# Optimization experiments

Hardware: AMD Instinct MI355X
Metric: run time of the kernel (lower is better)

## Reference

```python
import jax, jax.numpy as jnp
import numpy as np

B, T, D, KDIM = 256, 512, 256, 256

def setup_inputs() -> dict:
    key = jax.random.key(0)
    k1, k2, k3 = jax.random.split(key, 3)
    inputs = jax.random.normal(k1, (B, T, D), dtype=jnp.float32)
    # glorot-style scaling for stability of the recurrence
    U = jax.random.normal(k2, (D, KDIM), dtype=jnp.float32) * (1.0 / np.sqrt(D))
    W = jax.random.normal(k3, (KDIM, KDIM), dtype=jnp.float32) * (1.0 / np.sqrt(KDIM))
    b = jnp.zeros((KDIM,), dtype=jnp.float32)
    return {"inputs": inputs, "U": U, "W": W, "b": b}

def reference(inputs, U, W, b):
    # vanilla RNN: h_t = tanh(x_t U + h_{t-1} W + b); returns final hidden state
    xU = jnp.einsum('btd,dk->btk', inputs, U) + b  # precompute input projection [B,T,K]

    def step(h, xu_t):
        h = jnp.tanh(xu_t + h @ W)
        return h, None

    h0 = jnp.zeros((inputs.shape[0], W.shape[0]), dtype=inputs.dtype)
    h_final, _ = jax.lax.scan(step, h0, jnp.swapaxes(xU, 0, 1))  # scan over time
    # original keras code keeps a singleton time axis on the state: [B,1,K]
    return h_final[:, None, :]
```

## Files before the change

### kernel.cpp

```cpp
#include <hip/hip_runtime.h>
#include <hip/hip_bf16.h>


typedef _Float16 half8_t __attribute__((ext_vector_type(8)));
typedef _Float16 half2_t __attribute__((ext_vector_type(2)));
typedef float    float4_t __attribute__((ext_vector_type(4)));

#define MFMA16(a, b, c) __builtin_amdgcn_mfma_f32_16x16x32_f16((a), (b), (c), 0, 0, 0)

__device__ __forceinline__ half2_t pk_h2(float a, float b) {
    auto r = __builtin_amdgcn_cvt_pkrtz(a, b);
    return __builtin_bit_cast(half2_t, r);
}

__device__ __forceinline__ float fast_tanh(float x) {
    float e = __builtin_amdgcn_exp2f(2.8853900817779268f * x);
    return 1.0f - 2.0f * __builtin_amdgcn_rcpf(e + 1.0f);
}

__device__ __forceinline__ void lds_barrier() {
    __builtin_amdgcn_sched_barrier(0);
    asm volatile("s_waitcnt lgkmcnt(0)" ::: "memory");
    __builtin_amdgcn_s_barrier();
    __builtin_amdgcn_sched_barrier(0);
}

__global__ void transpose_u(const float* __restrict__ U, _Float16* __restrict__ Ut) {
    int id = blockIdx.x * 256 + threadIdx.x;
    int d = id >> 8, n = id & 255;
    Ut[n * 264 + d] = (_Float16)U[id];
}

__global__ __launch_bounds__(256, 2) void xu_gemm(
    const float* __restrict__ x,
    const _Float16* __restrict__ Ut,
    const float* __restrict__ bias,
    half2_t* __restrict__ xu)
{
    __shared__ char lds[61440];
    const int tid = threadIdx.x;
    const int lane = tid & 63, w = tid >> 6, l15 = lane & 15, q = lane >> 4;
    const int bx = blockIdx.x;
    const size_t m0 = (size_t)bx * 128;

    float4 ar[4];
    uint4  br[4];

    auto loadA = [&](int it) {
#pragma unroll
        for (int i = 0; i < 4; ++i) {
            int u = tid + 256 * i, row = u >> 3, seg = u & 7;
            ar[i] = *(const float4*)(x + (m0 + row) * 256 + it * 32 + seg * 4);
        }
    };
    auto loadB = [&](int it) {
#pragma unroll
        for (int i = 0; i < 4; ++i) {
            int u = tid + 256 * i, p = u >> 2, seg = u & 3;
            int c = 32 * (p >> 5) + 2 * (p & 15) + ((p >> 4) & 1);
            br[i] = *(const uint4*)((const char*)Ut + c * 528 + it * 64 + seg * 16);
        }
    };
    auto writeAB = [&](int s) {
        char* As = lds + s * 10240;
        char* Bs = lds + 20480 + s * 20480;
#pragma unroll
        for (int i = 0; i < 4; ++i) {
            int u = tid + 256 * i, row = u >> 3, seg = u & 7;
            half2_t p0 = pk_h2(ar[i].x, ar[i].y);
            half2_t p1 = pk_h2(ar[i].z, ar[i].w);
            uint2 v;
            v.x = __builtin_bit_cast(unsigned, p0);
            v.y = __builtin_bit_cast(unsigned, p1);
            *(uint2*)(As + row * 80 + seg * 8) = v;
        }
#pragma unroll
        for (int i = 0; i < 4; ++i) {
            int u = tid + 256 * i, p = u >> 2, seg = u & 3;
            *(uint4*)(Bs + p * 80 + seg * 16) = br[i];
        }
    };

    float4_t acc[32];
#pragma unroll
    for (int i = 0; i < 32; ++i) { acc[i][0] = 0.f; acc[i][1] = 0.f; acc[i][2] = 0.f; acc[i][3] = 0.f; }

    loadA(0); loadB(0); writeAB(0);
    __syncthreads();

    for (int it = 0; it < 8; ++it) {
        if (it < 7) { loadA(it + 1); loadB(it + 1); }
        const char* As = lds + (it & 1) * 10240;
        const char* Bs = lds + 20480 + (it & 1) * 20480;
        half8_t af[2];
#pragma unroll
        for (int ms = 0; ms < 2; ++ms)
            af[ms] = *(const half8_t*)(As + (32 * w + 16 * ms + l15) * 80 + q * 16);
#pragma unroll
        for (int ns = 0; ns < 16; ++ns) {
            half8_t bf = *(const half8_t*)(Bs + (16 * ns + l15) * 80 + q * 16);
            acc[ns * 2 + 0] = MFMA16(af[0], bf, acc[ns * 2 + 0]);
            acc[ns * 2 + 1] = MFMA16(af[1], bf, acc[ns * 2 + 1]);
        }
        if (it < 7) writeAB((it + 1) & 1);
        __syncthreads();
    }

#pragma unroll
    for (int ms = 0; ms < 2; ++ms)
#pragma unroll
        for (int j = 0; j < 8; ++j) {
            const int c = 32 * j + 2 * l15;
            const float2 bb = *(const float2*)(bias + c);
#pragma unroll
            for (int i = 0; i < 4; ++i) {
                float v0 = acc[(2 * j) * 2 + ms][i] + bb.x;
                float v1 = acc[(2 * j + 1) * 2 + ms][i] + bb.y;
                half2_t p = pk_h2(v0, v1);
                int m_g = bx * 128 + 32 * w + 16 * ms + q * 4 + i;
                xu[(size_t)m_g * 128 + (c >> 1)] = p;
            }
        }
}

__global__ __launch_bounds__(512, 2) void rnn_scan(
    const half2_t* __restrict__ xu,
    const float* __restrict__ W,
    float* __restrict__ out)
{
    __shared__ char lds[16896];
    const int tid = threadIdx.x;
    const int lane = tid & 63, w = tid >> 6, l15 = lane & 15, q = lane >> 4;
    const int blk = blockIdx.x;
    const int c0 = 32 * w + 2 * l15;

    half8_t wf[2][8];
#pragma unroll
    for (int tt = 0; tt < 2; ++tt)
#pragma unroll
        for (int c = 0; c < 8; ++c) {
            half8_t f;
#pragma unroll
            for (int j = 0; j < 8; ++j) {
                int k = 32 * c + q * 8 + j;
                f[j] = (_Float16)W[k * 256 + c0 + tt];
            }
            wf[tt][c] = f;
        }

    for (int i = tid; i < 16896 / 4; i += 512) ((int*)lds)[i] = 0;

    const int rowg0 = 16 * blk + q * 4;
    const int colh = c0 >> 1;

    half2_t xr[4][4];
#pragma unroll
    for (int p = 0; p < 4; ++p)
#pragma unroll
        for (int i = 0; i < 4; ++i)
            xr[p][i] = xu[((size_t)(rowg0 + i) * 512 + p) * 128 + colh];

    __syncthreads();

    char* const hbuf0 = (char*)lds;
    char* const hbuf1 = (char*)lds + 8448;

    for (int t4 = 0; t4 < 512; t4 += 4) {
#pragma unroll
        for (int p = 0; p < 4; ++p) {
            const int t = t4 + p;

            const char* hcur = (t & 1) ? hbuf1 : hbuf0;
            half8_t af[8];
#pragma unroll
            for (int c = 0; c < 8; ++c)
                af[c] = *(const half8_t*)(hcur + l15 * 528 + c * 64 + q * 16);

            float4_t a0a, a1a, a0b, a1b;
#pragma unroll
            for (int i = 0; i < 4; ++i) {
                a0a[i] = (float)xr[p][i][0];
                a1a[i] = (float)xr[p][i][1];
                a0b[i] = 0.f; a1b[i] = 0.f;
            }

            const int tn = (t + 4 <= 511) ? (t + 4) : 511;
#pragma unroll
            for (int i = 0; i < 4; ++i)
                xr[p][i] = xu[((size_t)(rowg0 + i) * 512 + tn) * 128 + colh];

#pragma unroll
            for (int c = 0; c < 4; ++c) {
                a0a = MFMA16(af[2 * c],     wf[0][2 * c],     a0a);
                a1a = MFMA16(af[2 * c],     wf[1][2 * c],     a1a);
                a0b = MFMA16(af[2 * c + 1], wf[0][2 * c + 1], a0b);
                a1b = MFMA16(af[2 * c + 1], wf[1][2 * c + 1], a1b);
            }

            if (t == 511) {
#pragma unroll
                for (int i = 0; i < 4; ++i) {
                    float v0 = fast_tanh(a0a[i] + a0b[i]);
                    float v1 = fast_tanh(a1a[i] + a1b[i]);
                    float2 st; st.x = v0; st.y = v1;
                    *(float2*)(&out[(rowg0 + i) * 256 + c0]) = st;
                }
            } else {
                char* hnext = ((t + 1) & 1) ? hbuf1 : hbuf0;
#pragma unroll
                for (int i = 0; i < 4; ++i) {
                    float v0 = fast_tanh(a0a[i] + a0b[i]);
                    float v1 = fast_tanh(a1a[i] + a1b[i]);
                    *(half2_t*)(hnext + (q * 4 + i) * 528 + c0 * 2) = pk_h2(v0, v1);
                }
            }
            lds_barrier();
        }
    }
}

extern "C" void kernel_launch(void* const* d_in, const int* in_sizes, int n_in,
                              void* d_out, int out_size, void* d_ws, size_t ws_size,
                              hipStream_t stream) {
    const float* x = (const float*)d_in[0];
    const float* U = (const float*)d_in[1];
    const float* W = (const float*)d_in[2];
    const float* b = (const float*)d_in[3];
    float* out = (float*)d_out;

    char* ws = (char*)d_ws;
    _Float16* Ut = (_Float16*)ws;
    half2_t*  xu = (half2_t*)(ws + 262144);

    transpose_u<<<256, 256, 0, stream>>>(U, Ut);
    xu_gemm<<<1024, 256, 0, stream>>>(x, Ut, b, xu);
    rnn_scan<<<16, 512, 0, stream>>>(xu, W, out);
}
```

Measured before the change: 521.1 us.

## Split RNN scan across 16 waves with one output column per lane

Doubles the scan block from 512 to 1024 threads, so each wave owns 16 output columns instead of 32. Each lane now computes a single column, which halves the MFMA chain per wave per timestep (4+4 instead of 8+8) and halves the W fragments held in registers. The aim is to shorten the serial per-step critical path of the recurrence. The cost is a barrier across twice as many waves each step, and narrower 16-bit LDS stores and xu loads.

After: 581.4 us. 1.12x slower.

```diff
diff --git a/kernel.cpp b/kernel.cpp
--- a/kernel.cpp
+++ b/kernel.cpp
@@ -123,8 +123,8 @@
         }
 }
 
-__global__ __launch_bounds__(512, 2) void rnn_scan(
-    const half2_t* __restrict__ xu,
+__global__ __launch_bounds__(1024, 4) void rnn_scan(
+    const _Float16* __restrict__ xu,
     const float* __restrict__ W,
     float* __restrict__ out)
 {
@@ -132,33 +132,30 @@
     const int tid = threadIdx.x;
     const int lane = tid & 63, w = tid >> 6, l15 = lane & 15, q = lane >> 4;
     const int blk = blockIdx.x;
-    const int c0 = 32 * w + 2 * l15;
-
-    half8_t wf[2][8];
-#pragma unroll
-    for (int tt = 0; tt < 2; ++tt)
-#pragma unroll
-        for (int c = 0; c < 8; ++c) {
-            half8_t f;
-#pragma unroll
-            for (int j = 0; j < 8; ++j) {
-                int k = 32 * c + q * 8 + j;
-                f[j] = (_Float16)W[k * 256 + c0 + tt];
-            }
-            wf[tt][c] = f;
-        }
-
-    for (int i = tid; i < 16896 / 4; i += 512) ((int*)lds)[i] = 0;
+    const int c = 16 * w + l15;
+
+    half8_t wf[8];
+#pragma unroll
+    for (int c8 = 0; c8 < 8; ++c8) {
+        half8_t f;
+#pragma unroll
+        for (int j = 0; j < 8; ++j) {
+            int k = 32 * c8 + q * 8 + j;
+            f[j] = (_Float16)W[k * 256 + c];
+        }
+        wf[c8] = f;
+    }
+
+    for (int i = tid; i < 16896 / 4; i += 1024) ((int*)lds)[i] = 0;
 
     const int rowg0 = 16 * blk + q * 4;
-    const int colh = c0 >> 1;
-
-    half2_t xr[4][4];
+
+    _Float16 xr[4][4];
 #pragma unroll
     for (int p = 0; p < 4; ++p)
 #pragma unroll
         for (int i = 0; i < 4; ++i)
-            xr[p][i] = xu[((size_t)(rowg0 + i) * 512 + p) * 128 + colh];
+            xr[p][i] = xu[((size_t)(rowg0 + i) * 512 + p) * 256 + c];
 
     __syncthreads();
 
@@ -173,45 +170,34 @@
             const char* hcur = (t & 1) ? hbuf1 : hbuf0;
             half8_t af[8];
 #pragma unroll
-            for (int c = 0; c < 8; ++c)
-                af[c] = *(const half8_t*)(hcur + l15 * 528 + c * 64 + q * 16);
-
-            float4_t a0a, a1a, a0b, a1b;
-#pragma unroll
-            for (int i = 0; i < 4; ++i) {
-                a0a[i] = (float)xr[p][i][0];
-                a1a[i] = (float)xr[p][i][1];
-                a0b[i] = 0.f; a1b[i] = 0.f;
+            for (int c8 = 0; c8 < 8; ++c8)
+                af[c8] = *(const half8_t*)(hcur + l15 * 528 + c8 * 64 + q * 16);
+
+            float4_t aA, aB;
+#pragma unroll
+            for (int i = 0; i < 4; ++i) { aA[i] = (float)xr[p][i]; aB[i] = 0.f; }
+
+            const int tn = (t + 4 <= 511) ? (t + 4) : 511;
+#pragma unroll
+            for (int i = 0; i < 4; ++i)
+                xr[p][i] = xu[((size_t)(rowg0 + i) * 512 + tn) * 256 + c];
+
+#pragma unroll
+            for (int c8 = 0; c8 < 4; ++c8) {
+                aA = MFMA16(af[2 * c8],     wf[2 * c8],     aA);
+                aB = MFMA16(af[2 * c8 + 1], wf[2 * c8 + 1], aB);
             }
 
-            const int tn = (t + 4 <= 511) ? (t + 4) : 511;
-#pragma unroll
-            for (int i = 0; i < 4; ++i)
-                xr[p][i] = xu[((size_t)(rowg0 + i) * 512 + tn) * 128 + colh];
-
-#pragma unroll
-            for (int c = 0; c < 4; ++c) {
-                a0a = MFMA16(af[2 * c],     wf[0][2 * c],     a0a);
-                a1a = MFMA16(af[2 * c],     wf[1][2 * c],     a1a);
-                a0b = MFMA16(af[2 * c + 1], wf[0][2 * c + 1], a0b);
-                a1b = MFMA16(af[2 * c + 1], wf[1][2 * c + 1], a1b);
-            }
-
             if (t == 511) {
 #pragma unroll
-                for (int i = 0; i < 4; ++i) {
-                    float v0 = fast_tanh(a0a[i] + a0b[i]);
-                    float v1 = fast_tanh(a1a[i] + a1b[i]);
-                    float2 st; st.x = v0; st.y = v1;
-                    *(float2*)(&out[(rowg0 + i) * 256 + c0]) = st;
-                }
+                for (int i = 0; i < 4; ++i)
+                    out[(rowg0 + i) * 256 + c] = fast_tanh(aA[i] + aB[i]);
             } else {
                 char* hnext = ((t + 1) & 1) ? hbuf1 : hbuf0;
 #pragma unroll
                 for (int i = 0; i < 4; ++i) {
-                    float v0 = fast_tanh(a0a[i] + a0b[i]);
-                    float v1 = fast_tanh(a1a[i] + a1b[i]);
-                    *(half2_t*)(hnext + (q * 4 + i) * 528 + c0 * 2) = pk_h2(v0, v1);
+                    float v = fast_tanh(aA[i] + aB[i]);
+                    *(_Float16*)(hnext + (q * 4 + i) * 528 + c * 2) = (_Float16)v;
                 }
             }
             lds_barrier();
@@ -234,5 +220,5 @@
 
     transpose_u<<<256, 256, 0, stream>>>(U, Ut);
     xu_gemm<<<1024, 256, 0, stream>>>(x, Ut, b, xu);
-    rnn_scan<<<16, 512, 0, stream>>>(xu, W, out);
-}
+    rnn_scan<<<16, 1024, 0, stream>>>((const _Float16*)xu, W, out);
+}
```
